# Performance work log

Measured on AMD Instinct MI355X. Metric: run time of the kernel, lower is better.

Reference implementation:

```python
import jax, jax.numpy as jnp
import numpy as np

# FusionTransformer with input_resolution=(1, 8192): window_size collapses to 1,
# shift_size forced to 0, attn_mask is None. Inside WindowAttention each window
# has N=1 token, so the 512-truncation and the stride-2 subsample are no-ops,
# softmax over a single key yields 1, and the attention output equals v.
# We still compute q/k, the scaled logit, the relative-position bias (index
# table is [[0]]) and the softmax faithfully.

B, L, C = 8, 8192, 384
NH, CS = 8, 3
DIN = C // CS              # 128 = dim // channel_scale
HD = C // NH // CS         # 16  = per-head qk/v dim
SCALE = (C // NH) ** -0.5  # uses head_dim = dim // num_heads = 48 (as in source)
HID = int(DIN * 4.0)       # 512 mlp hidden
EPS = 1e-5                 # torch LayerNorm default


def setup_inputs() -> dict:
    key = jax.random.key(0)
    ks = jax.random.split(key, 8)
    w = lambda k, shape: jax.random.normal(k, shape, jnp.float32) * 0.02
    return {
        "x": jax.random.normal(ks[0], (B, L, C), jnp.float32),
        "g1": jnp.ones((C,), jnp.float32), "b1": jnp.zeros((C,), jnp.float32),
        "Wq": w(ks[1], (C, DIN)), "bq": jnp.zeros((DIN,), jnp.float32),
        "Wkv": w(ks[2], (C, 2 * DIN)), "bkv": jnp.zeros((2 * DIN,), jnp.float32),
        "rpb": w(ks[3], (1, NH)),  # (2*ws-1)^2 = 1 table rows at ws=1
        "Wp": w(ks[4], (DIN, DIN)), "bp": jnp.zeros((DIN,), jnp.float32),
        "g2": jnp.ones((DIN,), jnp.float32), "b2": jnp.zeros((DIN,), jnp.float32),
        "W1": w(ks[5], (DIN, HID)), "bm1": jnp.zeros((HID,), jnp.float32),
        "W2": w(ks[6], (HID, DIN)), "bm2": jnp.zeros((DIN,), jnp.float32),
    }


def _ln(x, g, b):
    m = x.mean(-1, keepdims=True)
    v = ((x - m) ** 2).mean(-1, keepdims=True)
    return (x - m) * jax.lax.rsqrt(v + EPS) * g + b


def reference(x, g1, b1, Wq, bq, Wkv, bkv, rpb, Wp, bp, g2, b2, W1, bm1, W2, bm2):
    Bx, Lx, _ = x.shape
    h = _ln(x, g1, b1)                       # norm1
    # window partition with ws=1: every token is a (N=1) window; B_ = B*L.
    q = h @ Wq + bq                          # (B, L, DIN)
    kv = h @ Wkv + bkv                       # (B, L, 2*DIN); split dim-0 of the
    k, v = kv[..., :DIN], kv[..., DIN:]      # reshape(...,2,NH,HD) -> k, v
    qh = q.reshape(Bx, Lx, NH, HD)
    kh = k.reshape(Bx, Lx, NH, HD)
    vh = v.reshape(Bx, Lx, NH, HD)
    # attn logits (B, L, NH, 1, 1) flattened: q*scale . k + rel-pos bias[idx=0]
    logits = jnp.einsum('blhd,blhd->blh', qh * SCALE, kh) + rpb[0]
    attn = jax.nn.softmax(logits[..., None], axis=-1)   # softmax over N=1 keys
    out = (attn * vh).reshape(Bx, Lx, NH * HD)          # attn @ v, heads merged
    y = out @ Wp + bp                                   # proj
    # residual branch: x = attn_out; x = x + mlp(norm2(x))
    z = y + (jax.nn.gelu(_ln(y, g2, b2) @ W1 + bm1, approximate=False) @ W2 + bm2)
    return z
```

## Files before the change

### kernel.cpp

```cpp
#include <hip/hip_runtime.h>
#include <hip/hip_bf16.h>
#include <stdint.h>


typedef __attribute__((ext_vector_type(8))) short bf16x8;
typedef __attribute__((ext_vector_type(4))) float f32x4;

__device__ __forceinline__ short f2bf(float f) {
  union { float f; unsigned u; } a; a.f = f;
  unsigned u = a.u;
  u += 0x7fffu + ((u >> 16) & 1u);
  return (short)(u >> 16);
}
__device__ __forceinline__ float bf2f(short s) {
  union { unsigned u; float f; } a; a.u = ((unsigned)(unsigned short)s) << 16;
  return a.f;
}
__device__ __forceinline__ void gload_lds16(const void* g, void* l) {
  __builtin_amdgcn_global_load_lds(
      (const __attribute__((address_space(1))) unsigned*)g,
      (__attribute__((address_space(3))) unsigned*)l, 16, 0, 0);
}

__global__ void prep(const float* __restrict__ Wkv, const float* __restrict__ bkv,
                     const float* __restrict__ Wp,  const float* __restrict__ bp,
                     const float* __restrict__ W1,  const float* __restrict__ W2,
                     short* __restrict__ WcT, short* __restrict__ W1T,
                     short* __restrict__ W2T, float* __restrict__ bc) {
  const int b = blockIdx.x, tid = threadIdx.x;
  if (b < 192) {
    __shared__ float wv[2][128];
    const int kk = tid >> 7, n = tid & 127;
    wv[kk][n] = Wkv[(2 * b + kk) * 256 + 128 + n];
    __syncthreads();
    float s0 = 0, s1 = 0, s2 = 0, s3 = 0;
#pragma unroll 8
    for (int m = 0; m < 128; m += 4) {
      s0 += wv[kk][m]     * Wp[(m)     * 128 + n];
      s1 += wv[kk][m + 1] * Wp[(m + 1) * 128 + n];
      s2 += wv[kk][m + 2] * Wp[(m + 2) * 128 + n];
      s3 += wv[kk][m + 3] * Wp[(m + 3) * 128 + n];
    }
    WcT[n * 392 + (2 * b + kk)] = f2bf(s0 + s1 + s2 + s3);
  } else if (b == 192) {
    if (tid < 128) {
      float s = bp[tid];
#pragma unroll 8
      for (int m = 0; m < 128; ++m) s += bkv[128 + m] * Wp[m * 128 + tid];
      bc[tid] = s;
    }
  } else if (b < 449) {
    const int id = (b - 193) * 256 + tid;
    const int k = id >> 9, n = id & 511;
    W1T[n * 136 + k] = f2bf(W1[k * 512 + n]);
  } else {
    const int id = (b - 449) * 256 + tid;
    const int k = id >> 7, n = id & 127;
    W2T[(k >> 6) * 9216 + n * 72 + (k & 63)] = f2bf(W2[k * 128 + n]);
  }
}

__global__ __launch_bounds__(256)
void k1(const float* __restrict__ x,  const float* __restrict__ g1,
        const float* __restrict__ b1, const float* __restrict__ g2,
        const float* __restrict__ b2,
        const short* __restrict__ WcTg, const float* __restrict__ bcg,
        short* __restrict__ yb, short* __restrict__ lb) {
  __shared__ __align__(16) short WcT_l[128 * 392];
  __shared__ __align__(16) short A1[64 * 392];
  __shared__ float bcf[128], g2f[128], b2f[128];
  const int tid = threadIdx.x, lane = tid & 63, w = tid >> 6;
  const int q = lane >> 4, c16 = lane & 15, arow = w * 16 + c16;

  {
    const char* gsrc = (const char*)WcTg;
    for (int c = w; c < 98; c += 4)
      gload_lds16(gsrc + c * 1024 + lane * 16, (char*)WcT_l + c * 1024);
  }
  if (tid < 128) { bcf[tid] = bcg[tid]; g2f[tid] = g2[tid]; b2f[tid] = b2[tid]; }
  __syncthreads();

  for (int it = 0; it < 4; ++it) {
    const long tile = (long)blockIdx.x * 4 + it;
    const long tok0 = tile * 64;
    {
      const int row = tid >> 2, part = tid & 3;
      const float* xp = x + (tok0 + row) * 384 + part * 96;
      float4 xv[24]; float s = 0.f, sq = 0.f;
#pragma unroll
      for (int i = 0; i < 24; ++i) {
        float4 v = ((const float4*)xp)[i]; xv[i] = v;
        s += v.x + v.y + v.z + v.w;
        sq += v.x * v.x + v.y * v.y + v.z * v.z + v.w * v.w;
      }
      s += __shfl_xor(s, 1);  s += __shfl_xor(s, 2);
      sq += __shfl_xor(sq, 1); sq += __shfl_xor(sq, 2);
      const float mean = s * (1.f / 384.f);
      const float rs = rsqrtf(sq * (1.f / 384.f) - mean * mean + 1e-5f);
      const float4* g1p = (const float4*)(g1 + part * 96);
      const float4* b1p = (const float4*)(b1 + part * 96);
      short* dst = A1 + row * 392 + part * 96;
#pragma unroll
      for (int i = 0; i < 24; ++i) {
        float4 g = g1p[i], bb = b1p[i], v = xv[i]; short4 o;
        o.x = f2bf((v.x - mean) * rs * g.x + bb.x);
        o.y = f2bf((v.y - mean) * rs * g.y + bb.y);
        o.z = f2bf((v.z - mean) * rs * g.z + bb.z);
        o.w = f2bf((v.w - mean) * rs * g.w + bb.w);
        ((short4*)dst)[i] = o;
      }
    }
    __syncthreads();
    f32x4 yacc[8];
#pragma unroll
    for (int t = 0; t < 8; ++t) yacc[t] = (f32x4){0.f, 0.f, 0.f, 0.f};
#pragma unroll
    for (int ks = 0; ks < 12; ++ks) {
      bf16x8 af = *(const bf16x8*)(A1 + arow * 392 + ks * 32 + q * 8);
#pragma unroll
      for (int t = 0; t < 8; ++t) {
        bf16x8 bf = *(const bf16x8*)(WcT_l + (t * 16 + c16) * 392 + ks * 32 + q * 8);
        yacc[t] = __builtin_amdgcn_mfma_f32_16x16x32_bf16(af, bf, yacc[t], 0, 0, 0);
      }
    }
    float sm[4] = {0, 0, 0, 0}, sv[4] = {0, 0, 0, 0};
#pragma unroll
    for (int t = 0; t < 8; ++t) {
      const float bb = bcf[t * 16 + c16];
#pragma unroll
      for (int r = 0; r < 4; ++r) {
        yacc[t][r] += bb; const float v = yacc[t][r]; sm[r] += v; sv[r] += v * v;
      }
    }
#pragma unroll
    for (int r = 0; r < 4; ++r) {
      sm[r] += __shfl_xor(sm[r], 1); sm[r] += __shfl_xor(sm[r], 2);
      sm[r] += __shfl_xor(sm[r], 4); sm[r] += __shfl_xor(sm[r], 8);
      sv[r] += __shfl_xor(sv[r], 1); sv[r] += __shfl_xor(sv[r], 2);
      sv[r] += __shfl_xor(sv[r], 4); sv[r] += __shfl_xor(sv[r], 8);
    }
    short* ybp = yb + (tile * 4 + w) * 2048;
    short* lbp = lb + (tile * 4 + w) * 2048;
#pragma unroll
    for (int r = 0; r < 4; ++r) {
      const float mn = sm[r] * (1.f / 128.f);
      const float rv = rsqrtf(sv[r] * (1.f / 128.f) - mn * mn + 1e-5f);
#pragma unroll
      for (int t = 0; t < 8; ++t) {
        const int off = ((t * 4 + r) * 4 + q) * 16 + c16;
        const float yv = yacc[t][r];
        ybp[off] = f2bf(yv);
        lbp[off] = f2bf((yv - mn) * rv * g2f[t * 16 + c16] + b2f[t * 16 + c16]);
      }
    }
  }
}

__global__ __launch_bounds__(256)
void k2(const short* __restrict__ yb, const short* __restrict__ lb,
        const short* __restrict__ W1Tg, const short* __restrict__ W2Tg,
        const float* __restrict__ bm1, const float* __restrict__ bm2,
        float* __restrict__ out) {
  __shared__ __align__(16) short W1c[64 * 136];
  __shared__ __align__(16) short W2c[128 * 72];
  __shared__ __align__(16) short A3s[4][16 * 72];
  __shared__ float bm1f[512], bm2f[128];
  const int tid = threadIdx.x, lane = tid & 63, w = tid >> 6;
  const int q = lane >> 4, c16 = lane & 15;
  if (tid < 128) ((float4*)bm1f)[tid] = ((const float4*)bm1)[tid];
  else if (tid < 160) ((float4*)bm2f)[tid - 128] = ((const float4*)bm2)[tid - 128];

  const long tpair = blockIdx.x;
  bf16x8 a2[2][4];
#pragma unroll
  for (int u = 0; u < 2; ++u) {
    const short* base = lb + ((2 * tpair + u) * 4 + w) * 2048;
#pragma unroll
    for (int ks = 0; ks < 4; ++ks) {
      const int t = ks * 2 + (q >> 1);
      const int off = ((t * 4 + (c16 & 3)) * 4 + (c16 >> 2)) * 16 + (q & 1) * 8;
      a2[u][ks] = *(const bf16x8*)(base + off);
    }
  }
  f32x4 zacc[2][8];
#pragma unroll
  for (int u = 0; u < 2; ++u)
#pragma unroll
    for (int t = 0; t < 8; ++t) zacc[u][t] = (f32x4){0.f, 0.f, 0.f, 0.f};

  for (int ch = 0; ch < 8; ++ch) {
    const char* g1s = (const char*)W1Tg + ch * 17408;
    const char* g2s = (const char*)W2Tg + ch * 18432;
    for (int c = w; c < 17; c += 4) gload_lds16(g1s + c * 1024 + lane * 16, (char*)W1c + c * 1024);
    for (int c = w; c < 18; c += 4) gload_lds16(g2s + c * 1024 + lane * 16, (char*)W2c + c * 1024);
    __syncthreads();
#pragma unroll
    for (int u = 0; u < 2; ++u) {
      f32x4 hacc[4];
#pragma unroll
      for (int tt = 0; tt < 4; ++tt) hacc[tt] = (f32x4){0.f, 0.f, 0.f, 0.f};
#pragma unroll
      for (int ks = 0; ks < 4; ++ks)
#pragma unroll
        for (int tt = 0; tt < 4; ++tt) {
          bf16x8 bf = *(const bf16x8*)(W1c + (tt * 16 + c16) * 136 + ks * 32 + q * 8);
          hacc[tt] = __builtin_amdgcn_mfma_f32_16x16x32_bf16(a2[u][ks], bf, hacc[tt], 0, 0, 0);
        }
      short* a3 = A3s[w];
#pragma unroll
      for (int tt = 0; tt < 4; ++tt) {
        const float bb = bm1f[ch * 64 + tt * 16 + c16];
#pragma unroll
        for (int r = 0; r < 4; ++r) {
          const float h = hacc[tt][r] + bb;
          a3[(q * 4 + r) * 72 + tt * 16 + c16] =
              f2bf(0.5f * h * (1.f + erff(h * 0.70710678118f)));
        }
      }
      asm volatile("s_waitcnt lgkmcnt(0)" ::: "memory");
#pragma unroll
      for (int ks = 0; ks < 2; ++ks) {
        bf16x8 af = *(const bf16x8*)(a3 + c16 * 72 + ks * 32 + q * 8);
#pragma unroll
        for (int t = 0; t < 8; ++t) {
          bf16x8 bf = *(const bf16x8*)(W2c + (t * 16 + c16) * 72 + ks * 32 + q * 8);
          zacc[u][t] = __builtin_amdgcn_mfma_f32_16x16x32_bf16(af, bf, zacc[u][t], 0, 0, 0);
        }
      }
    }
    __syncthreads();
  }
#pragma unroll
  for (int u = 0; u < 2; ++u) {
    const long tile = 2 * tpair + u;
    const short* ybase = yb + (tile * 4 + w) * 2048;
#pragma unroll
    for (int t = 0; t < 8; ++t) {
      const float bb = bm2f[t * 16 + c16];
#pragma unroll
      for (int r = 0; r < 4; ++r) {
        const float yv = bf2f(ybase[((t * 4 + r) * 4 + q) * 16 + c16]);
        const long rowg = tile * 64 + w * 16 + q * 4 + r;
        out[rowg * 128 + t * 16 + c16] = yv + zacc[u][t][r] + bb;
      }
    }
  }
}

extern "C" void kernel_launch(void* const* d_in, const int* in_sizes, int n_in,
                              void* d_out, int out_size, void* d_ws, size_t ws_size,
                              hipStream_t stream) {
  const float* x   = (const float*)d_in[0];
  const float* g1  = (const float*)d_in[1];
  const float* b1  = (const float*)d_in[2];
  const float* Wkv = (const float*)d_in[5];
  const float* bkv = (const float*)d_in[6];
  const float* Wp  = (const float*)d_in[8];
  const float* bp  = (const float*)d_in[9];
  const float* g2  = (const float*)d_in[10];
  const float* b2  = (const float*)d_in[11];
  const float* W1  = (const float*)d_in[12];
  const float* bm1 = (const float*)d_in[13];
  const float* W2  = (const float*)d_in[14];
  const float* bm2 = (const float*)d_in[15];

  char* ws = (char*)d_ws;
  short* WcT = (short*)(ws + 0);
  short* W1T = (short*)(ws + 100352);
  short* W2T = (short*)(ws + 239616);
  float* bc  = (float*)(ws + 387072);
  short* yb  = (short*)(ws + 387584);
  short* lb  = (short*)(ws + 17164800);

  prep<<<705, 256, 0, stream>>>(Wkv, bkv, Wp, bp, W1, W2, WcT, W1T, W2T, bc);
  k1<<<256, 256, 0, stream>>>(x, g1, b1, g2, b2, WcT, bc, yb, lb);
  k2<<<512, 256, 0, stream>>>(yb, lb, W1T, W2T, bm1, bm2, (float*)d_out);
}
```

Before: 264.8 us.

## Keep LN1 fragments in registers, split MLP in two LDS-resident halves, fast GELU

k1 now runs 512 threads per block. Each wave builds its LayerNorm-1 bf16 MFMA A-fragments directly in registers instead of staging them through an LDS tile with a block barrier, and y is stored in a vectorised row layout. The MLP kernel is split into two launches, each holding half of W1/W2 fully in LDS. This removes the per-chunk weight reloads and barriers, but the partial residual sum is written back to the workspace as bf16 between the two passes. The exact erf GELU is replaced by an exp2/rcp sigmoid-style approximation, which adds bf16 rounding and approximation error, plus one extra launch and extra global traffic.

```diff
diff --git a/kernel.cpp b/kernel.cpp
--- a/kernel.cpp
+++ b/kernel.cpp
@@ -16,17 +16,26 @@
   union { unsigned u; float f; } a; a.u = ((unsigned)(unsigned short)s) << 16;
   return a.f;
 }
+__device__ __forceinline__ float gelu_fast(float h) {
+  float h2 = h * h;
+  float w  = h * (2.3022082f + 0.1029471f * h2);
+  float e  = __builtin_amdgcn_exp2f(w);
+  float r  = __builtin_amdgcn_rcpf(e + 1.0f);
+  return h - h * r;
+}
 __device__ __forceinline__ void gload_lds16(const void* g, void* l) {
   __builtin_amdgcn_global_load_lds(
       (const __attribute__((address_space(1))) unsigned*)g,
       (__attribute__((address_space(3))) unsigned*)l, 16, 0, 0);
 }
 
+
 __global__ void prep(const float* __restrict__ Wkv, const float* __restrict__ bkv,
                      const float* __restrict__ Wp,  const float* __restrict__ bp,
                      const float* __restrict__ W1,  const float* __restrict__ W2,
-                     short* __restrict__ WcT, short* __restrict__ W1T,
-                     short* __restrict__ W2T, float* __restrict__ bc) {
+                     short* __restrict__ WcT, short* __restrict__ W1Ta,
+                     short* __restrict__ W1Tb, short* __restrict__ W2Ta,
+                     short* __restrict__ W2Tb, float* __restrict__ bc) {
   const int b = blockIdx.x, tid = threadIdx.x;
   if (b < 192) {
     __shared__ float wv[2][128];
@@ -51,87 +60,104 @@
     }
   } else if (b < 449) {
     const int id = (b - 193) * 256 + tid;
-    const int k = id >> 9, n = id & 511;
-    W1T[n * 136 + k] = f2bf(W1[k * 512 + n]);
+    const int n = id & 511, k = id >> 9;
+    const short v = f2bf(W1[k * 512 + n]);
+    if (n < 256) W1Ta[n * 132 + k] = v;
+    else         W1Tb[(n - 256) * 132 + k] = v;
   } else {
     const int id = (b - 449) * 256 + tid;
-    const int k = id >> 7, n = id & 127;
-    W2T[(k >> 6) * 9216 + n * 72 + (k & 63)] = f2bf(W2[k * 128 + n]);
+    const int n = id & 127, k = id >> 7;
+    const int ch = k >> 6, kk = k & 63;
+    const short v = f2bf(W2[k * 128 + n]);
+    short* dst = (ch < 4) ? W2Ta : W2Tb;
+    dst[((ch & 3) * 128 + n) * 68 + kk] = v;
   }
 }
 
-__global__ __launch_bounds__(256)
+__global__ __launch_bounds__(512, 2)
 void k1(const float* __restrict__ x,  const float* __restrict__ g1,
         const float* __restrict__ b1, const float* __restrict__ g2,
         const float* __restrict__ b2,
         const short* __restrict__ WcTg, const float* __restrict__ bcg,
         short* __restrict__ yb, short* __restrict__ lb) {
   __shared__ __align__(16) short WcT_l[128 * 392];
-  __shared__ __align__(16) short A1[64 * 392];
-  __shared__ float bcf[128], g2f[128], b2f[128];
+  __shared__ __align__(16) float g1s[384], b1s[384], bcf[128], g2f[128], b2f[128];
   const int tid = threadIdx.x, lane = tid & 63, w = tid >> 6;
-  const int q = lane >> 4, c16 = lane & 15, arow = w * 16 + c16;
-
-  {
-    const char* gsrc = (const char*)WcTg;
-    for (int c = w; c < 98; c += 4)
-      gload_lds16(gsrc + c * 1024 + lane * 16, (char*)WcT_l + c * 1024);
+  const int q = lane >> 4, c16 = lane & 15;
+
+  for (int c = w; c < 98; c += 8)
+    gload_lds16((const char*)WcTg + c * 1024 + lane * 16, (char*)WcT_l + c * 1024);
+  if (tid < 96)       ((float4*)g1s)[tid]       = ((const float4*)g1)[tid];
+  else if (tid < 192) ((float4*)b1s)[tid - 96]  = ((const float4*)b1)[tid - 96];
+  else if (tid < 224) ((float4*)bcf)[tid - 192] = ((const float4*)bcg)[tid - 192];
+  else if (tid < 256) ((float4*)g2f)[tid - 224] = ((const float4*)g2)[tid - 224];
+  else if (tid < 288) ((float4*)b2f)[tid - 256] = ((const float4*)b2)[tid - 256];
+  __syncthreads();
+
+  float bcv[8], g2v[8], b2v[8];
+#pragma unroll
+  for (int t = 0; t < 8; ++t) {
+    bcv[t] = bcf[t * 16 + c16]; g2v[t] = g2f[t * 16 + c16]; b2v[t] = b2f[t * 16 + c16];
   }
-  if (tid < 128) { bcf[tid] = bcg[tid]; g2f[tid] = g2[tid]; b2f[tid] = b2[tid]; }
-  __syncthreads();
-
-  for (int it = 0; it < 4; ++it) {
-    const long tile = (long)blockIdx.x * 4 + it;
-    const long tok0 = tile * 64;
-    {
-      const int row = tid >> 2, part = tid & 3;
-      const float* xp = x + (tok0 + row) * 384 + part * 96;
-      float4 xv[24]; float s = 0.f, sq = 0.f;
-#pragma unroll
-      for (int i = 0; i < 24; ++i) {
-        float4 v = ((const float4*)xp)[i]; xv[i] = v;
-        s += v.x + v.y + v.z + v.w;
-        sq += v.x * v.x + v.y * v.y + v.z * v.z + v.w * v.w;
-      }
-      s += __shfl_xor(s, 1);  s += __shfl_xor(s, 2);
-      sq += __shfl_xor(sq, 1); sq += __shfl_xor(sq, 2);
-      const float mean = s * (1.f / 384.f);
-      const float rs = rsqrtf(sq * (1.f / 384.f) - mean * mean + 1e-5f);
-      const float4* g1p = (const float4*)(g1 + part * 96);
-      const float4* b1p = (const float4*)(b1 + part * 96);
-      short* dst = A1 + row * 392 + part * 96;
-#pragma unroll
-      for (int i = 0; i < 24; ++i) {
-        float4 g = g1p[i], bb = b1p[i], v = xv[i]; short4 o;
-        o.x = f2bf((v.x - mean) * rs * g.x + bb.x);
-        o.y = f2bf((v.y - mean) * rs * g.y + bb.y);
-        o.z = f2bf((v.z - mean) * rs * g.z + bb.z);
-        o.w = f2bf((v.w - mean) * rs * g.w + bb.w);
-        ((short4*)dst)[i] = o;
-      }
-    }
-    __syncthreads();
+
+  const int gw = blockIdx.x * 8 + w;
+  for (int i = 0; i < 2; ++i) {
+    const long band = (long)gw * 2 + i;
+    const float* xp = x + (band * 16 + c16) * 384 + q * 8;
+    float4 xa[24];
+#pragma unroll
+    for (int ks = 0; ks < 12; ++ks) {
+      xa[2 * ks]     = *(const float4*)(xp + ks * 32);
+      xa[2 * ks + 1] = *(const float4*)(xp + ks * 32 + 4);
+    }
+    float s = 0.f, sq = 0.f;
+#pragma unroll
+    for (int u = 0; u < 24; ++u) {
+      float4 v = xa[u];
+      s  += v.x + v.y + v.z + v.w;
+      sq += v.x * v.x + v.y * v.y + v.z * v.z + v.w * v.w;
+    }
+    s  += __shfl_xor(s, 16);  s  += __shfl_xor(s, 32);
+    sq += __shfl_xor(sq, 16); sq += __shfl_xor(sq, 32);
+    const float mean = s * (1.f / 384.f);
+    const float rs = rsqrtf(sq * (1.f / 384.f) - mean * mean + 1e-5f);
+    bf16x8 frag[12];
+#pragma unroll
+    for (int ks = 0; ks < 12; ++ks) {
+      const float4 ga = *(const float4*)(g1s + ks * 32 + q * 8);
+      const float4 gb = *(const float4*)(g1s + ks * 32 + q * 8 + 4);
+      const float4 ba = *(const float4*)(b1s + ks * 32 + q * 8);
+      const float4 bb = *(const float4*)(b1s + ks * 32 + q * 8 + 4);
+      const float4 va = xa[2 * ks], vb = xa[2 * ks + 1];
+      bf16x8 f;
+      f[0] = f2bf((va.x - mean) * rs * ga.x + ba.x);
+      f[1] = f2bf((va.y - mean) * rs * ga.y + ba.y);
+      f[2] = f2bf((va.z - mean) * rs * ga.z + ba.z);
+      f[3] = f2bf((va.w - mean) * rs * ga.w + ba.w);
+      f[4] = f2bf((vb.x - mean) * rs * gb.x + bb.x);
+      f[5] = f2bf((vb.y - mean) * rs * gb.y + bb.y);
+      f[6] = f2bf((vb.z - mean) * rs * gb.z + bb.z);
+      f[7] = f2bf((vb.w - mean) * rs * gb.w + bb.w);
+      frag[ks] = f;
+    }
     f32x4 yacc[8];
 #pragma unroll
     for (int t = 0; t < 8; ++t) yacc[t] = (f32x4){0.f, 0.f, 0.f, 0.f};
 #pragma unroll
-    for (int ks = 0; ks < 12; ++ks) {
-      bf16x8 af = *(const bf16x8*)(A1 + arow * 392 + ks * 32 + q * 8);
+    for (int ks = 0; ks < 12; ++ks)
 #pragma unroll
       for (int t = 0; t < 8; ++t) {
-        bf16x8 bf = *(const bf16x8*)(WcT_l + (t * 16 + c16) * 392 + ks * 32 + q * 8);
-        yacc[t] = __builtin_amdgcn_mfma_f32_16x16x32_bf16(af, bf, yacc[t], 0, 0, 0);
-      }
-    }
+        bf16x8 bfr = *(const bf16x8*)(WcT_l + (t * 16 + c16) * 392 + ks * 32 + q * 8);
+        yacc[t] = __builtin_amdgcn_mfma_f32_16x16x32_bf16(frag[ks], bfr, yacc[t], 0, 0, 0);
+      }
     float sm[4] = {0, 0, 0, 0}, sv[4] = {0, 0, 0, 0};
 #pragma unroll
-    for (int t = 0; t < 8; ++t) {
-      const float bb = bcf[t * 16 + c16];
+    for (int t = 0; t < 8; ++t)
 #pragma unroll
       for (int r = 0; r < 4; ++r) {
-        yacc[t][r] += bb; const float v = yacc[t][r]; sm[r] += v; sv[r] += v * v;
-      }
-    }
+        yacc[t][r] += bcv[t];
+        const float v = yacc[t][r]; sm[r] += v; sv[r] += v * v;
+      }
 #pragma unroll
     for (int r = 0; r < 4; ++r) {
       sm[r] += __shfl_xor(sm[r], 1); sm[r] += __shfl_xor(sm[r], 2);
@@ -139,63 +165,71 @@
       sv[r] += __shfl_xor(sv[r], 1); sv[r] += __shfl_xor(sv[r], 2);
       sv[r] += __shfl_xor(sv[r], 4); sv[r] += __shfl_xor(sv[r], 8);
     }
-    short* ybp = yb + (tile * 4 + w) * 2048;
-    short* lbp = lb + (tile * 4 + w) * 2048;
+    short* ybB = yb + band * 2048;
+    short* lbB = lb + band * 2048;
 #pragma unroll
     for (int r = 0; r < 4; ++r) {
       const float mn = sm[r] * (1.f / 128.f);
       const float rv = rsqrtf(sv[r] * (1.f / 128.f) - mn * mn + 1e-5f);
+      bf16x8 yp;
 #pragma unroll
       for (int t = 0; t < 8; ++t) {
-        const int off = ((t * 4 + r) * 4 + q) * 16 + c16;
         const float yv = yacc[t][r];
-        ybp[off] = f2bf(yv);
-        lbp[off] = f2bf((yv - mn) * rv * g2f[t * 16 + c16] + b2f[t * 16 + c16]);
-      }
+        yp[t] = f2bf(yv);
+        lbB[((t * 4 + r) * 4 + q) * 16 + c16] = f2bf((yv - mn) * rv * g2v[t] + b2v[t]);
+      }
+      *(bf16x8*)(ybB + ((r * 4 + q) * 16 + c16) * 8) = yp;
     }
   }
 }
 
-__global__ __launch_bounds__(256)
-void k2(const short* __restrict__ yb, const short* __restrict__ lb,
+template <bool FINAL>
+__global__ __launch_bounds__(512, 2)
+void k2(const short* __restrict__ lb, short* __restrict__ ybuf,
         const short* __restrict__ W1Tg, const short* __restrict__ W2Tg,
-        const float* __restrict__ bm1, const float* __restrict__ bm2,
+        const float* __restrict__ bm1h, const float* __restrict__ bm2,
         float* __restrict__ out) {
-  __shared__ __align__(16) short W1c[64 * 136];
-  __shared__ __align__(16) short W2c[128 * 72];
-  __shared__ __align__(16) short A3s[4][16 * 72];
-  __shared__ float bm1f[512], bm2f[128];
+  __shared__ __align__(16) short W1s[256 * 132];
+  __shared__ __align__(16) short W2s[4 * 128 * 68];
+  __shared__ __align__(16) short A3s[8][16 * 68];
+  __shared__ float bm1s[256], bm2s[128];
   const int tid = threadIdx.x, lane = tid & 63, w = tid >> 6;
   const int q = lane >> 4, c16 = lane & 15;
-  if (tid < 128) ((float4*)bm1f)[tid] = ((const float4*)bm1)[tid];
-  else if (tid < 160) ((float4*)bm2f)[tid - 128] = ((const float4*)bm2)[tid - 128];
-
-  const long tpair = blockIdx.x;
-  bf16x8 a2[2][4];
-#pragma unroll
-  for (int u = 0; u < 2; ++u) {
-    const short* base = lb + ((2 * tpair + u) * 4 + w) * 2048;
+
+  for (int c = w; c < 66; c += 8)
+    gload_lds16((const char*)W1Tg + c * 1024 + lane * 16, (char*)W1s + c * 1024);
+  for (int c = w; c < 68; c += 8)
+    gload_lds16((const char*)W2Tg + c * 1024 + lane * 16, (char*)W2s + c * 1024);
+  if (tid < 64) ((float4*)bm1s)[tid] = ((const float4*)bm1h)[tid];
+  else if (tid < 96) ((float4*)bm2s)[tid - 64] = ((const float4*)bm2)[tid - 64];
+  __syncthreads();
+
+  float bm2v[8];
+#pragma unroll
+  for (int t = 0; t < 8; ++t) bm2v[t] = bm2s[t * 16 + c16];
+
+  const int gw = blockIdx.x * 8 + w;
+  for (int i = 0; i < 2; ++i) {
+    const long band = (long)gw * 2 + i;
+    const short* lbB = lb + band * 2048;
+    short* ybB = ybuf + band * 2048;
+    bf16x8 a2f[4];
 #pragma unroll
     for (int ks = 0; ks < 4; ++ks) {
       const int t = ks * 2 + (q >> 1);
-      const int off = ((t * 4 + (c16 & 3)) * 4 + (c16 >> 2)) * 16 + (q & 1) * 8;
-      a2[u][ks] = *(const bf16x8*)(base + off);
-    }
-  }
-  f32x4 zacc[2][8];
-#pragma unroll
-  for (int u = 0; u < 2; ++u)
-#pragma unroll
-    for (int t = 0; t < 8; ++t) zacc[u][t] = (f32x4){0.f, 0.f, 0.f, 0.f};
-
-  for (int ch = 0; ch < 8; ++ch) {
-    const char* g1s = (const char*)W1Tg + ch * 17408;
-    const char* g2s = (const char*)W2Tg + ch * 18432;
-    for (int c = w; c < 17; c += 4) gload_lds16(g1s + c * 1024 + lane * 16, (char*)W1c + c * 1024);
-    for (int c = w; c < 18; c += 4) gload_lds16(g2s + c * 1024 + lane * 16, (char*)W2c + c * 1024);
-    __syncthreads();
-#pragma unroll
-    for (int u = 0; u < 2; ++u) {
+      a2f[ks] = *(const bf16x8*)(lbB + ((t * 4 + (c16 & 3)) * 4 + (c16 >> 2)) * 16 + (q & 1) * 8);
+    }
+    bf16x8 yf[4];
+#pragma unroll
+    for (int r = 0; r < 4; ++r)
+      yf[r] = *(const bf16x8*)(ybB + ((r * 4 + q) * 16 + c16) * 8);
+
+    f32x4 zacc[8];
+#pragma unroll
+    for (int t = 0; t < 8; ++t) zacc[t] = (f32x4){0.f, 0.f, 0.f, 0.f};
+
+#pragma unroll
+    for (int ch = 0; ch < 4; ++ch) {
       f32x4 hacc[4];
 #pragma unroll
       for (int tt = 0; tt < 4; ++tt) hacc[tt] = (f32x4){0.f, 0.f, 0.f, 0.f};
@@ -203,45 +237,45 @@
       for (int ks = 0; ks < 4; ++ks)
 #pragma unroll
         for (int tt = 0; tt < 4; ++tt) {
-          bf16x8 bf = *(const bf16x8*)(W1c + (tt * 16 + c16) * 136 + ks * 32 + q * 8);
-          hacc[tt] = __builtin_amdgcn_mfma_f32_16x16x32_bf16(a2[u][ks], bf, hacc[tt], 0, 0, 0);
+          bf16x8 bfr = *(const bf16x8*)(W1s + (ch * 64 + tt * 16 + c16) * 132 + ks * 32 + q * 8);
+          hacc[tt] = __builtin_amdgcn_mfma_f32_16x16x32_bf16(a2f[ks], bfr, hacc[tt], 0, 0, 0);
         }
       short* a3 = A3s[w];
 #pragma unroll
       for (int tt = 0; tt < 4; ++tt) {
-        const float bb = bm1f[ch * 64 + tt * 16 + c16];
+        const float bb = bm1s[ch * 64 + tt * 16 + c16];
 #pragma unroll
         for (int r = 0; r < 4; ++r) {
           const float h = hacc[tt][r] + bb;
-          a3[(q * 4 + r) * 72 + tt * 16 + c16] =
-              f2bf(0.5f * h * (1.f + erff(h * 0.70710678118f)));
+          a3[(q * 4 + r) * 68 + tt * 16 + c16] = f2bf(gelu_fast(h));
         }
       }
       asm volatile("s_waitcnt lgkmcnt(0)" ::: "memory");
 #pragma unroll
       for (int ks = 0; ks < 2; ++ks) {
-        bf16x8 af = *(const bf16x8*)(a3 + c16 * 72 + ks * 32 + q * 8);
+        bf16x8 af = *(const bf16x8*)(a3 + c16 * 68 + ks * 32 + q * 8);
 #pragma unroll
         for (int t = 0; t < 8; ++t) {
-          bf16x8 bf = *(const bf16x8*)(W2c + (t * 16 + c16) * 72 + ks * 32 + q * 8);
-          zacc[u][t] = __builtin_amdgcn_mfma_f32_16x16x32_bf16(af, bf, zacc[u][t], 0, 0, 0);
+          bf16x8 bfr = *(const bf16x8*)(W2s + (ch * 128 + t * 16 + c16) * 68 + ks * 32 + q * 8);
+          zacc[t] = __builtin_amdgcn_mfma_f32_16x16x32_bf16(af, bfr, zacc[t], 0, 0, 0);
         }
       }
     }
-    __syncthreads();
-  }
-#pragma unroll
-  for (int u = 0; u < 2; ++u) {
-    const long tile = 2 * tpair + u;
-    const short* ybase = yb + (tile * 4 + w) * 2048;
-#pragma unroll
-    for (int t = 0; t < 8; ++t) {
-      const float bb = bm2f[t * 16 + c16];
+    if (!FINAL) {
 #pragma unroll
       for (int r = 0; r < 4; ++r) {
-        const float yv = bf2f(ybase[((t * 4 + r) * 4 + q) * 16 + c16]);
-        const long rowg = tile * 64 + w * 16 + q * 4 + r;
-        out[rowg * 128 + t * 16 + c16] = yv + zacc[u][t][r] + bb;
+        bf16x8 zp;
+#pragma unroll
+        for (int t = 0; t < 8; ++t) zp[t] = f2bf(bf2f(yf[r][t]) + zacc[t][r]);
+        *(bf16x8*)(ybB + ((r * 4 + q) * 16 + c16) * 8) = zp;
+      }
+    } else {
+#pragma unroll
+      for (int r = 0; r < 4; ++r) {
+        const long rowg = band * 16 + q * 4 + r;
+#pragma unroll
+        for (int t = 0; t < 8; ++t)
+          out[rowg * 128 + t * 16 + c16] = bf2f(yf[r][t]) + zacc[t][r] + bm2v[t];
       }
     }
   }
@@ -265,14 +299,18 @@
   const float* bm2 = (const float*)d_in[15];
 
   char* ws = (char*)d_ws;
-  short* WcT = (short*)(ws + 0);
-  short* W1T = (short*)(ws + 100352);
-  short* W2T = (short*)(ws + 239616);
-  float* bc  = (float*)(ws + 387072);
-  short* yb  = (short*)(ws + 387584);
-  short* lb  = (short*)(ws + 17164800);
-
-  prep<<<705, 256, 0, stream>>>(Wkv, bkv, Wp, bp, W1, W2, WcT, W1T, W2T, bc);
-  k1<<<256, 256, 0, stream>>>(x, g1, b1, g2, b2, WcT, bc, yb, lb);
-  k2<<<512, 256, 0, stream>>>(yb, lb, W1T, W2T, bm1, bm2, (float*)d_out);
-}
+  short* WcT  = (short*)(ws + 0);
+  short* W1Ta = (short*)(ws + 100352);
+  short* W2Ta = (short*)(ws + 167936);
+  short* W1Tb = (short*)(ws + 237568);
+  short* W2Tb = (short*)(ws + 305152);
+  float* bc   = (float*)(ws + 374784);
+  short* ybuf = (short*)(ws + 376832);
+  short* lb   = (short*)(ws + 17154048);
+
+  prep<<<705, 256, 0, stream>>>(Wkv, bkv, Wp, bp, W1, W2,
+                                WcT, W1Ta, W1Tb, W2Ta, W2Tb, bc);
+  k1<<<256, 512, 0, stream>>>(x, g1, b1, g2, b2, WcT, bc, ybuf, lb);
+  k2<false><<<256, 512, 0, stream>>>(lb, ybuf, W1Ta, W2Ta, bm1, bm2, (float*)d_out);
+  k2<true><<<256, 512, 0, stream>>>(lb, ybuf, W1Tb, W2Tb, bm1 + 256, bm2, (float*)d_out);
+}
```

New measurement: 438.0 us. 1.65x slower.
